# Kernel tuning notes

Hardware: AMD Instinct MI355X
Metric: run time of the kernel (lower is better)

## Reference

```python
import jax, jax.numpy as jnp
import numpy as np

H = 1024   # hidden_size (== embedding dim)
V = 512    # output_size (vocab)
L = 2      # n_layers
T = 256    # max_length
B = 256    # batch
FP = 2048  # fingerprint dim (input to `connection` linear)


def setup_inputs() -> dict:
    key = jax.random.key(0)
    ks = jax.random.split(key, 12)
    s = 0.02
    return {
        "encoder_outputs": jax.random.normal(ks[0], (B, 1, H), jnp.float32),
        "fingerprints": jax.random.uniform(ks[1], (B, FP), jnp.float32),
        "target_tensor": jax.random.randint(ks[2], (B, T), 0, V),
        "emb": jax.random.normal(ks[3], (V, H), jnp.float32) * s,
        "Wc": jax.random.normal(ks[4], (H, FP), jnp.float32) * s,
        "bc": jnp.zeros((H,), jnp.float32),
        "W_ih": jax.random.normal(ks[5], (L, 3 * H, H), jnp.float32) * s,
        "W_hh": jax.random.normal(ks[6], (L, 3 * H, H), jnp.float32) * s,
        "b_ih": jnp.zeros((L, 3 * H), jnp.float32),
        "b_hh": jnp.zeros((L, 3 * H), jnp.float32),
        "Wo": jax.random.normal(ks[7], (V, H), jnp.float32) * s,
        "bo": jnp.zeros((V,), jnp.float32),
    }


def _gru_decode(tokens_tb, h0, emb, W_ih, W_hh, b_ih, b_hh, Wo, bo):
    # tokens_tb: [T,B] int; h0: [L,B,H]
    n_layers = W_ih.shape[0]

    def step(h, tok):
        x = jax.nn.relu(emb[tok])  # [B,H] (embedding lookup + relu)
        new_h = []
        inp = x
        for l in range(n_layers):  # small fixed layer count
            hl = h[l]
            gi = inp @ W_ih[l].T + b_ih[l]          # [B,3H]
            gh = hl @ W_hh[l].T + b_hh[l]           # [B,3H]
            i_r, i_z, i_n = jnp.split(gi, 3, axis=-1)
            h_r, h_z, h_n = jnp.split(gh, 3, axis=-1)
            r = jax.nn.sigmoid(i_r + h_r)
            z = jax.nn.sigmoid(i_z + h_z)
            n = jnp.tanh(i_n + r * h_n)
            hl = (1.0 - z) * n + z * hl
            new_h.append(hl)
            inp = hl
        out = inp @ Wo.T + bo  # [B,V]
        return jnp.stack(new_h), out

    h_final, outs = jax.lax.scan(step, h0, tokens_tb)  # outs: [T,B,V]
    return outs, h_final


def reference(encoder_outputs, fingerprints, target_tensor, emb, Wc, bc,
              W_ih, W_hh, b_ih, b_hh, Wo, bo):
    batch = encoder_outputs.shape[0]
    n_layers = W_ih.shape[0]
    # z = relu(connection(fingerprints)); hidden = stack(n_layers * [z])
    z = jax.nn.relu(fingerprints @ Wc.T + bc)            # [B,H]
    h0 = jnp.broadcast_to(z[None], (n_layers, batch, z.shape[-1]))
    # teacher forcing: input at step 0 is token 0, then target[:, i]
    tokens = jnp.concatenate(
        [jnp.zeros((batch, 1), target_tensor.dtype), target_tensor[:, :-1]], axis=1)
    outs, h_final = _gru_decode(tokens.T, h0, emb, W_ih, W_hh, b_ih, b_hh, Wo, bo)
    logits = jnp.transpose(outs, (1, 0, 2))              # [B,T,V]
    log_probs = jax.nn.log_softmax(logits, axis=-1)
    return log_probs, h_final
```

## Files before the change

### kernel.cpp

```cpp
#include <hip/hip_runtime.h>
#include <hip/hip_bf16.h>

#define HDIM 1024
#define VDIM 512
#define TLEN 256
#define BATCH 256
#define FPDIM 2048
#define H3 3072

typedef __hip_bfloat16 bf16;
typedef __attribute__((ext_vector_type(8))) short s8v;
typedef __attribute__((ext_vector_type(4))) float f4v;

__device__ __forceinline__ f4v mfma_bf16(s8v a, s8v b, f4v c) {
  return __builtin_amdgcn_mfma_f32_16x16x32_bf16(a, b, c, 0, 0, 0);
}
__device__ __forceinline__ s8v ld8(const bf16* p) { return *(const s8v*)p; }
__device__ __forceinline__ float sigf(float x) { return 1.f / (1.f + expf(-x)); }
__device__ __forceinline__ short f2bs(float f) {
  union { float f; unsigned u; } c; c.f = f;
  unsigned u = c.u + 0x7fff + ((c.u >> 16) & 1);
  return (short)(u >> 16);
}

__global__ __launch_bounds__(256) void shuffle_w(const float* __restrict__ src,
                                                 bf16* __restrict__ dst, int ngroups) {
  int g = blockIdx.x * 256 + threadIdx.x;
  if (g >= ngroups) return;
  int lane = g & 63, kc = (g >> 6) & 31, nt = g >> 11;
  int n = nt * 16 + (lane & 15);
  int k = kc * 32 + ((lane >> 4) << 3);
  const float* s = src + (size_t)n * HDIM + k;
  short* d = (short*)dst + (size_t)g * 8;
  s8v v;
#pragma unroll
  for (int j = 0; j < 8; ++j) v[j] = f2bs(s[j]);
  *(s8v*)d = v;
}

struct GemmArgs {
  const float* A; const float* W; const float* bias; const float* bias2;
  float* C; int ldc; int K; int reluA; int reluC; int b2lim;
};
#define LDP 68
__global__ __launch_bounds__(256) void gemm_bt(GemmArgs g) {
  __shared__ float As[16][LDP];
  __shared__ float Ws[16][LDP];
  const int tid = threadIdx.x;
  const int tx = tid & 15, ty = tid >> 4;
  const int m0 = blockIdx.y * 64, n0 = blockIdx.x * 64;
  float acc[4][4] = {{0.f, 0.f, 0.f, 0.f}};
  const int K = g.K;
  for (int kb = 0; kb < K / 16; ++kb) {
    const int k0 = kb * 16;
#pragma unroll
    for (int i = 0; i < 4; ++i) {
      int idx = tid + i * 256;
      int ml = idx >> 4, kl = idx & 15;
      float a = g.A[(size_t)(m0 + ml) * K + k0 + kl];
      if (g.reluA) a = fmaxf(a, 0.f);
      As[kl][ml] = a;
      Ws[kl][ml] = g.W[(size_t)(n0 + ml) * K + k0 + kl];
    }
    __syncthreads();
#pragma unroll
    for (int k = 0; k < 16; ++k) {
      float4 av = *(const float4*)&As[k][ty * 4];
      float4 wv = *(const float4*)&Ws[k][tx * 4];
      float a[4] = {av.x, av.y, av.z, av.w};
      float w[4] = {wv.x, wv.y, wv.z, wv.w};
#pragma unroll
      for (int i = 0; i < 4; ++i)
#pragma unroll
        for (int j = 0; j < 4; ++j)
          acc[i][j] = fmaf(a[i], w[j], acc[i][j]);
    }
    __syncthreads();
  }
#pragma unroll
  for (int i = 0; i < 4; ++i) {
    int m = m0 + ty * 4 + i;
#pragma unroll
    for (int j = 0; j < 4; ++j) {
      int n = n0 + tx * 4 + j;
      float v = acc[i][j] + g.bias[n];
      if (g.bias2 && n < g.b2lim) v += g.bias2[n];
      if (g.reluC) v = fmaxf(v, 0.f);
      g.C[(size_t)m * g.ldc + n] = v;
    }
  }
}

__global__ __launch_bounds__(256) void copy2(const float* __restrict__ s,
                                             float* __restrict__ d0,
                                             float* __restrict__ d1) {
  int i = blockIdx.x * 256 + threadIdx.x;
  float v = s[i];
  d0[i] = v; d1[i] = v;
}

__global__ __launch_bounds__(256) void permute_frag(const float* __restrict__ s,
                                                    bf16* __restrict__ d0,
                                                    bf16* __restrict__ d1) {
  int g = blockIdx.x * 256 + threadIdx.x;
  int lane = g & 63, kc = (g >> 6) & 31, mt = g >> 11;
  int m = mt * 16 + (lane & 15), k = kc * 32 + ((lane >> 4) << 3);
  const float* src = s + (size_t)m * HDIM + k;
  s8v v;
#pragma unroll
  for (int j = 0; j < 8; ++j) v[j] = f2bs(src[j]);
  *(s8v*)((short*)d0 + (size_t)g * 8) = v;
  *(s8v*)((short*)d1 + (size_t)g * 8) = v;
}

struct StepArgs {
  int k;
  const int* target;
  const float* table;
  const bf16* Whh0;
  const float* bhh0n;
  const bf16* h0f_in; const float* h0l_in;
  bf16* h0f_out;      float* h0l_out;
  const bf16* Wih1; const bf16* Whh1;
  const float* bih1; const float* bhh1;
  const bf16* h1f_in; const float* h1l_in;
  bf16* h1f_out;      float* h1l_out;
  const bf16* Wof; const float* bo;
  float* out;
};

__global__ __launch_bounds__(256) void step_fused(StepArgs g) {
  __shared__ float smax[4][16];
  __shared__ float ssum[4][16];
  const int blk = blockIdx.x;
  const int tid = threadIdx.x;
  const int w = tid >> 6, ln = tid & 63, l15 = ln & 15, quad = ln >> 4;

  if (blk < 64) {
    if (g.k > 255) return;
    const int mg = blk >> 4, ng = blk & 15;
    const int wy = w >> 1, wx = w & 1;
    const int mbase = mg * 64 + wy * 32;
    const int nbase = ng * 64 + wx * 32;
    const int MT0 = mbase >> 4;
    const int NT0 = nbase >> 4;
    int ncol[2]; float bhn[2];
#pragma unroll
    for (int nj = 0; nj < 2; ++nj) {
      ncol[nj] = nbase + nj * 16 + l15;
      bhn[nj] = g.bhh0n[ncol[nj]];
    }
    float tr_[2][2][4], tz_[2][2][4], tn_[2][2][4], hp[2][2][4];
#pragma unroll
    for (int mi = 0; mi < 2; ++mi)
#pragma unroll
      for (int r = 0; r < 4; ++r) {
        const int m = ((MT0 + mi) << 4) + (quad << 2) + r;
        const int tok = (g.k == 0) ? 0 : g.target[m * TLEN + g.k - 1];
        const float* trow = g.table + (size_t)tok * H3;
#pragma unroll
        for (int nj = 0; nj < 2; ++nj) {
          const int n = ncol[nj];
          tr_[mi][nj][r] = trow[n];
          tz_[mi][nj][r] = trow[n + 1024];
          tn_[mi][nj][r] = trow[n + 2048];
          hp[mi][nj][r] = g.h0l_in[(size_t)m * HDIM + n];
        }
      }
    const bf16* pA0 = g.h0f_in + ((size_t)MT0 * 32) * 512 + ln * 8;
    const bf16* pB[3][2];
#pragma unroll
    for (int gi = 0; gi < 3; ++gi)
#pragma unroll
      for (int nj = 0; nj < 2; ++nj)
        pB[gi][nj] = g.Whh0 + ((size_t)((gi << 6) + NT0 + nj) * 32) * 512 + ln * 8;
    const f4v z4 = {0.f, 0.f, 0.f, 0.f};
    f4v acc[3][2][2];
#pragma unroll
    for (int gi = 0; gi < 3; ++gi)
#pragma unroll
      for (int mi = 0; mi < 2; ++mi)
#pragma unroll
        for (int nj = 0; nj < 2; ++nj) acc[gi][mi][nj] = z4;
#pragma unroll 4
    for (int kc = 0; kc < 32; ++kc) {
      s8v A0 = ld8(pA0 + kc * 512);
      s8v A1 = ld8(pA0 + (32 * 512) + kc * 512);
#pragma unroll
      for (int gi = 0; gi < 3; ++gi)
#pragma unroll
        for (int nj = 0; nj < 2; ++nj) {
          s8v B = ld8(pB[gi][nj] + kc * 512);
          acc[gi][0][nj] = mfma_bf16(A0, B, acc[gi][0][nj]);
          acc[gi][1][nj] = mfma_bf16(A1, B, acc[gi][1][nj]);
        }
    }
    const int kc2 = nbase >> 5;
#pragma unroll
    for (int mi = 0; mi < 2; ++mi) {
      const int MT = MT0 + mi;
      short* fo = (short*)g.h0f_out + (((size_t)(MT * 32 + kc2)) << 9) + (l15 & 7);
#pragma unroll
      for (int r = 0; r < 4; ++r) {
        const int m = (MT << 4) + (quad << 2) + r;
#pragma unroll
        for (int nj = 0; nj < 2; ++nj) {
          const int n = ncol[nj];
          float rr = sigf(tr_[mi][nj][r] + acc[0][mi][nj][r]);
          float zz = sigf(tz_[mi][nj][r] + acc[1][mi][nj][r]);
          float nn = tanhf(tn_[mi][nj][r] + rr * (acc[2][mi][nj][r] + bhn[nj]));
          float hv = (1.f - zz) * nn + zz * hp[mi][nj][r];
          g.h0l_out[(size_t)m * HDIM + n] = hv;
          const int lanep = (quad << 2) + r + (((nj << 1) + (l15 >> 3)) << 4);
          fo[lanep * 8] = f2bs(hv);
        }
      }
    }
  } else if (blk < 192) {
    if (g.k < 1 || g.k > 256) return;
    const int b1 = blk - 64;
    const int mg = b1 >> 5, ng = b1 & 31;
    const int my = w >> 1, ny = w & 1;
    const int mbase = mg * 64 + my * 32;
    const int nbase = ng * 32 + ny * 16;
    const int MT0 = mbase >> 4;
    const int NT = nbase >> 4;
    const int n = nbase + l15;
    const float br = g.bih1[n] + g.bhh1[n];
    const float bz = g.bih1[n + 1024] + g.bhh1[n + 1024];
    const float bin = g.bih1[n + 2048], bhn = g.bhh1[n + 2048];
    float hp[2][4];
#pragma unroll
    for (int mi = 0; mi < 2; ++mi)
#pragma unroll
      for (int r = 0; r < 4; ++r) {
        const int m = ((MT0 + mi) << 4) + (quad << 2) + r;
        hp[mi][r] = g.h1l_in[(size_t)m * HDIM + n];
      }
    const bf16* pAx = g.h0f_in + ((size_t)MT0 * 32) * 512 + ln * 8;
    const bf16* pAh = g.h1f_in + ((size_t)MT0 * 32) * 512 + ln * 8;
    const bf16* pI[3]; const bf16* pH[3];
#pragma unroll
    for (int gi = 0; gi < 3; ++gi) {
      pI[gi] = g.Wih1 + ((size_t)((gi << 6) + NT) * 32) * 512 + ln * 8;
      pH[gi] = g.Whh1 + ((size_t)((gi << 6) + NT) * 32) * 512 + ln * 8;
    }
    const f4v z4 = {0.f, 0.f, 0.f, 0.f};
    f4v ar[2] = {z4, z4}, az[2] = {z4, z4}, ain[2] = {z4, z4}, ahn[2] = {z4, z4};
#pragma unroll 2
    for (int kc = 0; kc < 32; ++kc) {
      s8v Ax0 = ld8(pAx + kc * 512);
      s8v Ax1 = ld8(pAx + (32 * 512) + kc * 512);
      s8v Ah0 = ld8(pAh + kc * 512);
      s8v Ah1 = ld8(pAh + (32 * 512) + kc * 512);
      s8v Bir = ld8(pI[0] + kc * 512);
      s8v Bhr = ld8(pH[0] + kc * 512);
      s8v Biz = ld8(pI[1] + kc * 512);
      s8v Bhz = ld8(pH[1] + kc * 512);
      s8v Bin = ld8(pI[2] + kc * 512);
      s8v Bhn = ld8(pH[2] + kc * 512);
      ar[0] = mfma_bf16(Ax0, Bir, ar[0]);  ar[0] = mfma_bf16(Ah0, Bhr, ar[0]);
      ar[1] = mfma_bf16(Ax1, Bir, ar[1]);  ar[1] = mfma_bf16(Ah1, Bhr, ar[1]);
      az[0] = mfma_bf16(Ax0, Biz, az[0]);  az[0] = mfma_bf16(Ah0, Bhz, az[0]);
      az[1] = mfma_bf16(Ax1, Biz, az[1]);  az[1] = mfma_bf16(Ah1, Bhz, az[1]);
      ain[0] = mfma_bf16(Ax0, Bin, ain[0]);
      ain[1] = mfma_bf16(Ax1, Bin, ain[1]);
      ahn[0] = mfma_bf16(Ah0, Bhn, ahn[0]);
      ahn[1] = mfma_bf16(Ah1, Bhn, ahn[1]);
    }
    const int lhigh = (ny << 1) + (l15 >> 3);
#pragma unroll
    for (int mi = 0; mi < 2; ++mi) {
      const int MT = MT0 + mi;
      short* fo = (short*)g.h1f_out + (((size_t)(MT * 32 + ng)) << 9) + (l15 & 7);
#pragma unroll
      for (int r = 0; r < 4; ++r) {
        const int m = (MT << 4) + (quad << 2) + r;
        float rr = sigf(ar[mi][r] + br);
        float zz = sigf(az[mi][r] + bz);
        float nn = tanhf(ain[mi][r] + bin + rr * (ahn[mi][r] + bhn));
        float hv = (1.f - zz) * nn + zz * hp[mi][r];
        g.h1l_out[(size_t)m * HDIM + n] = hv;
        fo[((quad << 2) + r + (lhigh << 4)) * 8] = f2bs(hv);
      }
    }
  } else {
    if (g.k < 2) return;
    const int to = g.k - 2;
    const int blk2 = blk - 192;
    const int MT = blk2;
    const bf16* pA = g.h1f_in + ((size_t)MT * 32) * 512 + ln * 8;
    float bov[8];
#pragma unroll
    for (int u = 0; u < 8; ++u) bov[u] = g.bo[(w << 7) + (u << 4) + l15];
    const f4v z4 = {0.f, 0.f, 0.f, 0.f};
    f4v acc[8];
#pragma unroll
    for (int u = 0; u < 8; ++u) acc[u] = z4;
#pragma unroll 2
    for (int kc = 0; kc < 32; ++kc) {
      s8v A = ld8(pA + kc * 512);
#pragma unroll
      for (int u = 0; u < 8; ++u) {
        s8v B = ld8(g.Wof + (((size_t)((w << 3) + u) * 32 + kc) << 9) + ln * 8);
        acc[u] = mfma_bf16(A, B, acc[u]);
      }
    }
    float lg[8][4];
#pragma unroll
    for (int u = 0; u < 8; ++u)
#pragma unroll
      for (int r = 0; r < 4; ++r) lg[u][r] = acc[u][r] + bov[u];
    float mx[4];
#pragma unroll
    for (int r = 0; r < 4; ++r) {
      float m0 = lg[0][r];
#pragma unroll
      for (int u = 1; u < 8; ++u) m0 = fmaxf(m0, lg[u][r]);
#pragma unroll
      for (int o = 8; o > 0; o >>= 1) m0 = fmaxf(m0, __shfl_xor(m0, o));
      mx[r] = m0;
    }
    if (l15 == 0) {
#pragma unroll
      for (int r = 0; r < 4; ++r) smax[w][(quad << 2) + r] = mx[r];
    }
    __syncthreads();
    float rm[4];
#pragma unroll
    for (int r = 0; r < 4; ++r) {
      float m0 = smax[0][(quad << 2) + r];
#pragma unroll
      for (int ww = 1; ww < 4; ++ww) m0 = fmaxf(m0, smax[ww][(quad << 2) + r]);
      rm[r] = m0;
    }
    float sm[4];
#pragma unroll
    for (int r = 0; r < 4; ++r) {
      float s0 = 0.f;
#pragma unroll
      for (int u = 0; u < 8; ++u) s0 += expf(lg[u][r] - rm[r]);
#pragma unroll
      for (int o = 8; o > 0; o >>= 1) s0 += __shfl_xor(s0, o);
      sm[r] = s0;
    }
    if (l15 == 0) {
#pragma unroll
      for (int r = 0; r < 4; ++r) ssum[w][(quad << 2) + r] = sm[r];
    }
    __syncthreads();
#pragma unroll
    for (int r = 0; r < 4; ++r) {
      float s0 = ssum[0][(quad << 2) + r];
#pragma unroll
      for (int ww = 1; ww < 4; ++ww) s0 += ssum[ww][(quad << 2) + r];
      const float lse = rm[r] + logf(s0);
      const int m = (MT << 4) + (quad << 2) + r;
      float* orow = g.out + ((size_t)m * TLEN + to) * VDIM;
#pragma unroll
      for (int u = 0; u < 8; ++u) orow[(w << 7) + (u << 4) + l15] = lg[u][r] - lse;
    }
  }
}

__global__ __launch_bounds__(256) void unperm_hfinal(const float* __restrict__ h0l,
                                                     const float* __restrict__ h1l,
                                                     float* __restrict__ out) {
  int idx = blockIdx.x * 256 + threadIdx.x;
  const int BH = BATCH * HDIM;
  out[idx] = (idx < BH) ? h0l[idx] : h1l[idx - BH];
}

extern "C" void kernel_launch(void* const* d_in, const int* in_sizes, int n_in,
                              void* d_out, int out_size, void* d_ws, size_t ws_size,
                              hipStream_t stream) {
  const float* fps    = (const float*)d_in[1];
  const int* target   = (const int*)d_in[2];
  const float* emb    = (const float*)d_in[3];
  const float* Wc     = (const float*)d_in[4];
  const float* bc     = (const float*)d_in[5];
  const float* W_ih   = (const float*)d_in[6];
  const float* W_hh   = (const float*)d_in[7];
  const float* b_ih   = (const float*)d_in[8];
  const float* b_hh   = (const float*)d_in[9];
  const float* Wo     = (const float*)d_in[10];
  const float* bo     = (const float*)d_in[11];
  float* out = (float*)d_out;

  const int BH = BATCH * HDIM;
  const size_t WN = (size_t)H3 * HDIM;

  char* p = (char*)d_ws;
  float* hstd  = (float*)p; p += (size_t)BH * 4;
  float* table = (float*)p; p += (size_t)VDIM * H3 * 4;
  float* H0l[2]; H0l[0] = (float*)p; p += (size_t)BH * 4; H0l[1] = (float*)p; p += (size_t)BH * 4;
  float* H1l[2]; H1l[0] = (float*)p; p += (size_t)BH * 4; H1l[1] = (float*)p; p += (size_t)BH * 4;
  bf16* H0f[2]; H0f[0] = (bf16*)p; p += (size_t)BH * 2; H0f[1] = (bf16*)p; p += (size_t)BH * 2;
  bf16* H1f[2]; H1f[0] = (bf16*)p; p += (size_t)BH * 2; H1f[1] = (bf16*)p; p += (size_t)BH * 2;
  bf16* Whh0f = (bf16*)p; p += WN * 2;
  bf16* Wih1f = (bf16*)p; p += WN * 2;
  bf16* Whh1f = (bf16*)p; p += WN * 2;
  bf16* Wof   = (bf16*)p; p += (size_t)VDIM * HDIM * 2;

  {
    int ng3 = (H3 / 16) * 32 * 64;
    shuffle_w<<<ng3 / 256, 256, 0, stream>>>(W_hh, Whh0f, ng3);
    shuffle_w<<<ng3 / 256, 256, 0, stream>>>(W_ih + WN, Wih1f, ng3);
    shuffle_w<<<ng3 / 256, 256, 0, stream>>>(W_hh + WN, Whh1f, ng3);
    int ngv = (VDIM / 16) * 32 * 64;
    shuffle_w<<<ngv / 256, 256, 0, stream>>>(Wo, Wof, ngv);
  }
  {
    GemmArgs a; a.A = fps; a.W = Wc; a.bias = bc; a.bias2 = nullptr;
    a.C = hstd; a.ldc = HDIM; a.K = FPDIM; a.reluA = 0; a.reluC = 1; a.b2lim = 0;
    gemm_bt<<<dim3(HDIM / 64, BATCH / 64), 256, 0, stream>>>(a);
  }
  {
    GemmArgs a; a.A = emb; a.W = W_ih; a.bias = b_ih; a.bias2 = b_hh;
    a.C = table; a.ldc = H3; a.K = HDIM; a.reluA = 1; a.reluC = 0; a.b2lim = 2048;
    gemm_bt<<<dim3(H3 / 64, VDIM / 64), 256, 0, stream>>>(a);
  }
  copy2<<<BH / 256, 256, 0, stream>>>(hstd, H0l[0], H1l[0]);
  permute_frag<<<(BATCH / 16) * 32 * 64 / 256, 256, 0, stream>>>(hstd, H0f[0], H1f[0]);

  for (int k = 0; k <= TLEN + 1; ++k) {
    StepArgs s;
    s.k = k; s.target = target; s.table = table;
    s.Whh0 = Whh0f; s.bhh0n = b_hh + 2048;
    s.h0f_in = H0f[k & 1];         s.h0l_in = H0l[k & 1];
    s.h0f_out = H0f[(k + 1) & 1];  s.h0l_out = H0l[(k + 1) & 1];
    s.Wih1 = Wih1f; s.Whh1 = Whh1f;
    s.bih1 = b_ih + H3; s.bhh1 = b_hh + H3;
    s.h1f_in = H1f[(k + 1) & 1];   s.h1l_in = H1l[(k + 1) & 1];
    s.h1f_out = H1f[k & 1];        s.h1l_out = H1l[k & 1];
    s.Wof = Wof; s.bo = bo; s.out = out;
    step_fused<<<208, 256, 0, stream>>>(s);
  }

  unperm_hfinal<<<2 * BH / 256, 256, 0, stream>>>(H0l[0], H1l[0],
                                                  out + (size_t)BATCH * TLEN * VDIM);
}
```

Measured before the change: 6.091 ms.

## Split K across wave pairs with LDS exchange, doubling block to 512 threads

Each block of the fused GRU step kernel now runs 8 waves instead of 4. The extra waves split the reduction dimension (layer 0 and the output projection) or the input-vs-hidden GEMM (layer 1). Partial accumulators are exchanged through shared memory so each wave finalizes half the rows. This doubles the wavefronts working per step on a latency-bound 208-block launch, which should shorten each sequential step's critical path. The cost is an LDS round trip, a barrier, and higher shared-memory use per block.

```diff
diff --git a/kernel.cpp b/kernel.cpp
--- a/kernel.cpp
+++ b/kernel.cpp
@@ -129,9 +129,12 @@
   float* out;
 };
 
-__global__ __launch_bounds__(256) void step_fused(StepArgs g) {
-  __shared__ float smax[4][16];
-  __shared__ float ssum[4][16];
+#define EXP 25
+
+__global__ __launch_bounds__(512, 2) void step_fused(StepArgs g) {
+  __shared__ float exch[8][64][EXP];
+  __shared__ float smax[8][16];
+  __shared__ float ssum[8][16];
   const int blk = blockIdx.x;
   const int tid = threadIdx.x;
   const int w = tid >> 6, ln = tid & 63, l15 = ln & 15, quad = ln >> 4;
@@ -139,34 +142,33 @@
   if (blk < 64) {
     if (g.k > 255) return;
     const int mg = blk >> 4, ng = blk & 15;
-    const int wy = w >> 1, wx = w & 1;
+    const int wx = w & 1, wy = (w >> 1) & 1, kh = w >> 2;
     const int mbase = mg * 64 + wy * 32;
     const int nbase = ng * 64 + wx * 32;
     const int MT0 = mbase >> 4;
     const int NT0 = nbase >> 4;
+    const int MTe = MT0 + kh;
     int ncol[2]; float bhn[2];
 #pragma unroll
     for (int nj = 0; nj < 2; ++nj) {
       ncol[nj] = nbase + nj * 16 + l15;
       bhn[nj] = g.bhh0n[ncol[nj]];
     }
-    float tr_[2][2][4], tz_[2][2][4], tn_[2][2][4], hp[2][2][4];
-#pragma unroll
-    for (int mi = 0; mi < 2; ++mi)
-#pragma unroll
-      for (int r = 0; r < 4; ++r) {
-        const int m = ((MT0 + mi) << 4) + (quad << 2) + r;
-        const int tok = (g.k == 0) ? 0 : g.target[m * TLEN + g.k - 1];
-        const float* trow = g.table + (size_t)tok * H3;
-#pragma unroll
-        for (int nj = 0; nj < 2; ++nj) {
-          const int n = ncol[nj];
-          tr_[mi][nj][r] = trow[n];
-          tz_[mi][nj][r] = trow[n + 1024];
-          tn_[mi][nj][r] = trow[n + 2048];
-          hp[mi][nj][r] = g.h0l_in[(size_t)m * HDIM + n];
-        }
+    float tr_[2][4], tz_[2][4], tn_[2][4], hp[2][4];
+#pragma unroll
+    for (int r = 0; r < 4; ++r) {
+      const int m = (MTe << 4) + (quad << 2) + r;
+      const int tok = (g.k == 0) ? 0 : g.target[m * TLEN + g.k - 1];
+      const float* trow = g.table + (size_t)tok * H3;
+#pragma unroll
+      for (int nj = 0; nj < 2; ++nj) {
+        const int n = ncol[nj];
+        tr_[nj][r] = trow[n];
+        tz_[nj][r] = trow[n + 1024];
+        tn_[nj][r] = trow[n + 2048];
+        hp[nj][r] = g.h0l_in[(size_t)m * HDIM + n];
       }
+    }
     const bf16* pA0 = g.h0f_in + ((size_t)MT0 * 32) * 512 + ln * 8;
     const bf16* pB[3][2];
 #pragma unroll
@@ -182,8 +184,9 @@
       for (int mi = 0; mi < 2; ++mi)
 #pragma unroll
         for (int nj = 0; nj < 2; ++nj) acc[gi][mi][nj] = z4;
+    const int kc0 = kh << 4;
 #pragma unroll 4
-    for (int kc = 0; kc < 32; ++kc) {
+    for (int kc = kc0; kc < kc0 + 16; ++kc) {
       s8v A0 = ld8(pA0 + kc * 512);
       s8v A1 = ld8(pA0 + (32 * 512) + kc * 512);
 #pragma unroll
@@ -195,128 +198,146 @@
           acc[gi][1][nj] = mfma_bf16(A1, B, acc[gi][1][nj]);
         }
     }
+    float* ex = &exch[w][ln][0];
+#pragma unroll
+    for (int gi = 0; gi < 3; ++gi)
+#pragma unroll
+      for (int nj = 0; nj < 2; ++nj)
+#pragma unroll
+        for (int r = 0; r < 4; ++r)
+          ex[(gi * 2 + nj) * 4 + r] = acc[gi][1 ^ kh][nj][r];
+    __syncthreads();
+    const float* px = &exch[w ^ 4][ln][0];
     const int kc2 = nbase >> 5;
-#pragma unroll
-    for (int mi = 0; mi < 2; ++mi) {
-      const int MT = MT0 + mi;
-      short* fo = (short*)g.h0f_out + (((size_t)(MT * 32 + kc2)) << 9) + (l15 & 7);
-#pragma unroll
-      for (int r = 0; r < 4; ++r) {
-        const int m = (MT << 4) + (quad << 2) + r;
-#pragma unroll
-        for (int nj = 0; nj < 2; ++nj) {
-          const int n = ncol[nj];
-          float rr = sigf(tr_[mi][nj][r] + acc[0][mi][nj][r]);
-          float zz = sigf(tz_[mi][nj][r] + acc[1][mi][nj][r]);
-          float nn = tanhf(tn_[mi][nj][r] + rr * (acc[2][mi][nj][r] + bhn[nj]));
-          float hv = (1.f - zz) * nn + zz * hp[mi][nj][r];
-          g.h0l_out[(size_t)m * HDIM + n] = hv;
-          const int lanep = (quad << 2) + r + (((nj << 1) + (l15 >> 3)) << 4);
-          fo[lanep * 8] = f2bs(hv);
-        }
+    short* fo = (short*)g.h0f_out + (((size_t)(MTe * 32 + kc2)) << 9) + (l15 & 7);
+#pragma unroll
+    for (int r = 0; r < 4; ++r) {
+      const int m = (MTe << 4) + (quad << 2) + r;
+#pragma unroll
+      for (int nj = 0; nj < 2; ++nj) {
+        const int n = ncol[nj];
+        const float a0 = acc[0][kh][nj][r] + px[(0 * 2 + nj) * 4 + r];
+        const float a1 = acc[1][kh][nj][r] + px[(1 * 2 + nj) * 4 + r];
+        const float a2 = acc[2][kh][nj][r] + px[(2 * 2 + nj) * 4 + r];
+        float rr = sigf(tr_[nj][r] + a0);
+        float zz = sigf(tz_[nj][r] + a1);
+        float nn = tanhf(tn_[nj][r] + rr * (a2 + bhn[nj]));
+        float hv = (1.f - zz) * nn + zz * hp[nj][r];
+        g.h0l_out[(size_t)m * HDIM + n] = hv;
+        const int lanep = (quad << 2) + r + (((nj << 1) + (l15 >> 3)) << 4);
+        fo[lanep * 8] = f2bs(hv);
       }
     }
   } else if (blk < 192) {
     if (g.k < 1 || g.k > 256) return;
     const int b1 = blk - 64;
     const int mg = b1 >> 5, ng = b1 & 31;
-    const int my = w >> 1, ny = w & 1;
+    const int ny = w & 1, my = (w >> 1) & 1, srcw = w >> 2;
     const int mbase = mg * 64 + my * 32;
     const int nbase = ng * 32 + ny * 16;
     const int MT0 = mbase >> 4;
     const int NT = nbase >> 4;
     const int n = nbase + l15;
+    const int MTe = MT0 + srcw;
     const float br = g.bih1[n] + g.bhh1[n];
     const float bz = g.bih1[n + 1024] + g.bhh1[n + 1024];
     const float bin = g.bih1[n + 2048], bhn = g.bhh1[n + 2048];
-    float hp[2][4];
-#pragma unroll
-    for (int mi = 0; mi < 2; ++mi)
-#pragma unroll
-      for (int r = 0; r < 4; ++r) {
-        const int m = ((MT0 + mi) << 4) + (quad << 2) + r;
-        hp[mi][r] = g.h1l_in[(size_t)m * HDIM + n];
+    float hp[4];
+#pragma unroll
+    for (int r = 0; r < 4; ++r) {
+      const int m = (MTe << 4) + (quad << 2) + r;
+      hp[r] = g.h1l_in[(size_t)m * HDIM + n];
+    }
+    const bf16* pA = (srcw ? g.h1f_in : g.h0f_in) + ((size_t)MT0 * 32) * 512 + ln * 8;
+    const bf16* Wsrc = srcw ? g.Whh1 : g.Wih1;
+    const bf16* pB[3];
+#pragma unroll
+    for (int gi = 0; gi < 3; ++gi)
+      pB[gi] = Wsrc + ((size_t)((gi << 6) + NT) * 32) * 512 + ln * 8;
+    const f4v z4 = {0.f, 0.f, 0.f, 0.f};
+    f4v acc[3][2];
+#pragma unroll
+    for (int gi = 0; gi < 3; ++gi) { acc[gi][0] = z4; acc[gi][1] = z4; }
+#pragma unroll 4
+    for (int kc = 0; kc < 32; ++kc) {
+      s8v A0 = ld8(pA + kc * 512);
+      s8v A1 = ld8(pA + (32 * 512) + kc * 512);
+#pragma unroll
+      for (int gi = 0; gi < 3; ++gi) {
+        s8v B = ld8(pB[gi] + kc * 512);
+        acc[gi][0] = mfma_bf16(A0, B, acc[gi][0]);
+        acc[gi][1] = mfma_bf16(A1, B, acc[gi][1]);
       }
-    const bf16* pAx = g.h0f_in + ((size_t)MT0 * 32) * 512 + ln * 8;
-    const bf16* pAh = g.h1f_in + ((size_t)MT0 * 32) * 512 + ln * 8;
-    const bf16* pI[3]; const bf16* pH[3];
-#pragma unroll
-    for (int gi = 0; gi < 3; ++gi) {
-      pI[gi] = g.Wih1 + ((size_t)((gi << 6) + NT) * 32) * 512 + ln * 8;
-      pH[gi] = g.Whh1 + ((size_t)((gi << 6) + NT) * 32) * 512 + ln * 8;
-    }
-    const f4v z4 = {0.f, 0.f, 0.f, 0.f};
-    f4v ar[2] = {z4, z4}, az[2] = {z4, z4}, ain[2] = {z4, z4}, ahn[2] = {z4, z4};
-#pragma unroll 2
-    for (int kc = 0; kc < 32; ++kc) {
-      s8v Ax0 = ld8(pAx + kc * 512);
-      s8v Ax1 = ld8(pAx + (32 * 512) + kc * 512);
-      s8v Ah0 = ld8(pAh + kc * 512);
-      s8v Ah1 = ld8(pAh + (32 * 512) + kc * 512);
-      s8v Bir = ld8(pI[0] + kc * 512);
-      s8v Bhr = ld8(pH[0] + kc * 512);
-      s8v Biz = ld8(pI[1] + kc * 512);
-      s8v Bhz = ld8(pH[1] + kc * 512);
-      s8v Bin = ld8(pI[2] + kc * 512);
-      s8v Bhn = ld8(pH[2] + kc * 512);
-      ar[0] = mfma_bf16(Ax0, Bir, ar[0]);  ar[0] = mfma_bf16(Ah0, Bhr, ar[0]);
-      ar[1] = mfma_bf16(Ax1, Bir, ar[1]);  ar[1] = mfma_bf16(Ah1, Bhr, ar[1]);
-      az[0] = mfma_bf16(Ax0, Biz, az[0]);  az[0] = mfma_bf16(Ah0, Bhz, az[0]);
-      az[1] = mfma_bf16(Ax1, Biz, az[1]);  az[1] = mfma_bf16(Ah1, Bhz, az[1]);
-      ain[0] = mfma_bf16(Ax0, Bin, ain[0]);
-      ain[1] = mfma_bf16(Ax1, Bin, ain[1]);
-      ahn[0] = mfma_bf16(Ah0, Bhn, ahn[0]);
-      ahn[1] = mfma_bf16(Ah1, Bhn, ahn[1]);
-    }
+    }
+    float* ex = &exch[w][ln][0];
+#pragma unroll
+    for (int gi = 0; gi < 3; ++gi)
+#pragma unroll
+      for (int r = 0; r < 4; ++r)
+        ex[gi * 4 + r] = acc[gi][1 ^ srcw][r];
+    __syncthreads();
+    const float* px = &exch[w ^ 4][ln][0];
     const int lhigh = (ny << 1) + (l15 >> 3);
-#pragma unroll
-    for (int mi = 0; mi < 2; ++mi) {
-      const int MT = MT0 + mi;
-      short* fo = (short*)g.h1f_out + (((size_t)(MT * 32 + ng)) << 9) + (l15 & 7);
-#pragma unroll
-      for (int r = 0; r < 4; ++r) {
-        const int m = (MT << 4) + (quad << 2) + r;
-        float rr = sigf(ar[mi][r] + br);
-        float zz = sigf(az[mi][r] + bz);
-        float nn = tanhf(ain[mi][r] + bin + rr * (ahn[mi][r] + bhn));
-        float hv = (1.f - zz) * nn + zz * hp[mi][r];
-        g.h1l_out[(size_t)m * HDIM + n] = hv;
-        fo[((quad << 2) + r + (lhigh << 4)) * 8] = f2bs(hv);
-      }
+    short* fo = (short*)g.h1f_out + (((size_t)(MTe * 32 + ng)) << 9) + (l15 & 7);
+#pragma unroll
+    for (int r = 0; r < 4; ++r) {
+      const int m = (MTe << 4) + (quad << 2) + r;
+      const float o0 = acc[0][srcw][r], p0 = px[0 * 4 + r];
+      const float o1 = acc[1][srcw][r], p1 = px[1 * 4 + r];
+      const float o2 = acc[2][srcw][r], p2 = px[2 * 4 + r];
+      const float xin = srcw ? p2 : o2;
+      const float hnn = srcw ? o2 : p2;
+      float rr = sigf(o0 + p0 + br);
+      float zz = sigf(o1 + p1 + bz);
+      float nn = tanhf(xin + bin + rr * (hnn + bhn));
+      float hv = (1.f - zz) * nn + zz * hp[r];
+      g.h1l_out[(size_t)m * HDIM + n] = hv;
+      fo[((quad << 2) + r + (lhigh << 4)) * 8] = f2bs(hv);
     }
   } else {
     if (g.k < 2) return;
     const int to = g.k - 2;
-    const int blk2 = blk - 192;
-    const int MT = blk2;
+    const int MT = blk - 192;
+    const int wn = w & 3, kh = w >> 2;
     const bf16* pA = g.h1f_in + ((size_t)MT * 32) * 512 + ln * 8;
-    float bov[8];
-#pragma unroll
-    for (int u = 0; u < 8; ++u) bov[u] = g.bo[(w << 7) + (u << 4) + l15];
+    float bov[4];
+#pragma unroll
+    for (int u = 0; u < 4; ++u)
+      bov[u] = g.bo[wn * 128 + kh * 64 + u * 16 + l15];
     const f4v z4 = {0.f, 0.f, 0.f, 0.f};
     f4v acc[8];
 #pragma unroll
     for (int u = 0; u < 8; ++u) acc[u] = z4;
+    const int kc0 = kh << 4;
 #pragma unroll 2
-    for (int kc = 0; kc < 32; ++kc) {
+    for (int kc = kc0; kc < kc0 + 16; ++kc) {
       s8v A = ld8(pA + kc * 512);
 #pragma unroll
       for (int u = 0; u < 8; ++u) {
-        s8v B = ld8(g.Wof + (((size_t)((w << 3) + u) * 32 + kc) << 9) + ln * 8);
+        s8v B = ld8(g.Wof + (((size_t)((wn << 3) + u) * 32 + kc) << 9) + ln * 8);
         acc[u] = mfma_bf16(A, B, acc[u]);
       }
     }
-    float lg[8][4];
-#pragma unroll
-    for (int u = 0; u < 8; ++u)
-#pragma unroll
-      for (int r = 0; r < 4; ++r) lg[u][r] = acc[u][r] + bov[u];
+    float* ex = &exch[w][ln][0];
+#pragma unroll
+    for (int u = 0; u < 4; ++u)
+#pragma unroll
+      for (int r = 0; r < 4; ++r)
+        ex[u * 4 + r] = acc[(1 ^ kh) * 4 + u][r];
+    __syncthreads();
+    const float* px = &exch[w ^ 4][ln][0];
+    float lg[4][4];
+#pragma unroll
+    for (int u = 0; u < 4; ++u)
+#pragma unroll
+      for (int r = 0; r < 4; ++r)
+        lg[u][r] = acc[kh * 4 + u][r] + px[u * 4 + r] + bov[u];
     float mx[4];
 #pragma unroll
     for (int r = 0; r < 4; ++r) {
       float m0 = lg[0][r];
 #pragma unroll
-      for (int u = 1; u < 8; ++u) m0 = fmaxf(m0, lg[u][r]);
+      for (int u = 1; u < 4; ++u) m0 = fmaxf(m0, lg[u][r]);
 #pragma unroll
       for (int o = 8; o > 0; o >>= 1) m0 = fmaxf(m0, __shfl_xor(m0, o));
       mx[r] = m0;
@@ -331,7 +352,7 @@
     for (int r = 0; r < 4; ++r) {
       float m0 = smax[0][(quad << 2) + r];
 #pragma unroll
-      for (int ww = 1; ww < 4; ++ww) m0 = fmaxf(m0, smax[ww][(quad << 2) + r]);
+      for (int ww = 1; ww < 8; ++ww) m0 = fmaxf(m0, smax[ww][(quad << 2) + r]);
       rm[r] = m0;
     }
     float sm[4];
@@ -339,7 +360,7 @@
     for (int r = 0; r < 4; ++r) {
       float s0 = 0.f;
 #pragma unroll
-      for (int u = 0; u < 8; ++u) s0 += expf(lg[u][r] - rm[r]);
+      for (int u = 0; u < 4; ++u) s0 += expf(lg[u][r] - rm[r]);
 #pragma unroll
       for (int o = 8; o > 0; o >>= 1) s0 += __shfl_xor(s0, o);
       sm[r] = s0;
@@ -353,12 +374,13 @@
     for (int r = 0; r < 4; ++r) {
       float s0 = ssum[0][(quad << 2) + r];
 #pragma unroll
-      for (int ww = 1; ww < 4; ++ww) s0 += ssum[ww][(quad << 2) + r];
+      for (int ww = 1; ww < 8; ++ww) s0 += ssum[ww][(quad << 2) + r];
       const float lse = rm[r] + logf(s0);
       const int m = (MT << 4) + (quad << 2) + r;
       float* orow = g.out + ((size_t)m * TLEN + to) * VDIM;
 #pragma unroll
-      for (int u = 0; u < 8; ++u) orow[(w << 7) + (u << 4) + l15] = lg[u][r] - lse;
+      for (int u = 0; u < 4; ++u)
+        orow[wn * 128 + kh * 64 + u * 16 + l15] = lg[u][r] - lse;
     }
   }
 }
@@ -434,7 +456,7 @@
     s.h1f_in = H1f[(k + 1) & 1];   s.h1l_in = H1l[(k + 1) & 1];
     s.h1f_out = H1f[k & 1];        s.h1l_out = H1l[k & 1];
     s.Wof = Wof; s.bo = bo; s.out = out;
-    step_fused<<<208, 256, 0, stream>>>(s);
+    step_fused<<<208, 512, 0, stream>>>(s);
   }
 
   unperm_hfinal<<<2 * BH / 256, 256, 0, stream>>>(H0l[0], H1l[0],
```

Result: slower. 6.317 ms (+3.7%).
